# Kernel tuning notes

Measured on AMD Instinct MI355X. Metric: run time of the kernel, lower is better.

Reference implementation:

```python
import jax, jax.numpy as jnp
import numpy as np

N = 50000        # num nodes
E = 800000       # num edges (avg degree 16)
IN_DIM = 64
OUT_DIM = 64
PE_DIM = 24
HEADS = 2
HID = OUT_DIM * HEADS  # 128


def setup_inputs() -> dict:
    key = jax.random.key(0)
    ks = jax.random.split(key, 16)
    std = 0.1  # trunc_normal_(std=0.1) init in the torch module
    return {
        "x": jax.random.normal(ks[0], (N, IN_DIM), jnp.float32),
        "pe_index": jax.random.randint(ks[1], (2, E), 0, N, jnp.int32),
        "pe_val": jax.random.normal(ks[2], (E, PE_DIM), jnp.float32),
        # edge-weight MLP (blocks): input proj, one residual FFN block, final proj
        "W_in": jax.random.normal(ks[3], (PE_DIM, HID), jnp.float32) * std,
        "b_in": jnp.zeros((HID,), jnp.float32),
        "W1": jax.random.normal(ks[4], (HID, HID), jnp.float32) * std,
        "b1": jnp.zeros((HID,), jnp.float32),
        "W2": jax.random.normal(ks[5], (HID, HID), jnp.float32) * std,
        "b2": jnp.zeros((HID,), jnp.float32),
        "W_fin": jax.random.normal(ks[6], (HID, HID), jnp.float32) * std,
        "b_fin": jnp.zeros((HID,), jnp.float32),
        # node feature -> multi-head projection
        "W_x": jax.random.normal(ks[7], (IN_DIM, HID), jnp.float32) * std,
        "b_x": jnp.zeros((HID,), jnp.float32),
        # per-head output bias
        "head_bias": jnp.zeros((1, HEADS, OUT_DIM), jnp.float32),
        # final out projection
        "W_out": jax.random.normal(ks[8], (HID, OUT_DIM), jnp.float32) * std,
        "b_out": jnp.zeros((OUT_DIM,), jnp.float32),
    }


def _edge_mlp(pe, W_in, b_in, W1, b1, W2, b2, W_fin, b_fin):
    # Linear(pe_dim->hid), then residual block [GELU, Linear, GELU, Linear, +res], then Linear(hid->hid)
    g = lambda t: jax.nn.gelu(t, approximate=False)  # torch nn.GELU default = exact erf
    x0 = pe @ W_in + b_in                     # [E, HID]
    h = g(x0) @ W1 + b1
    h = g(h) @ W2 + b2
    x0 = h + x0                               # ResidualLayer: x + x_res
    return x0 @ W_fin + b_fin                 # [E, HID]


def reference(x, pe_index, pe_val, W_in, b_in, W1, b1, W2, b2, W_fin, b_fin,
              W_x, b_x, head_bias, W_out, b_out):
    tgt = pe_index[0]  # messages aggregate to edge_index[0]
    src = pe_index[1]
    score = _edge_mlp(pe_val, W_in, b_in, W1, b1, W2, b2, W_fin, b_fin)
    score = score.reshape(-1, HEADS, OUT_DIM)                 # [E, H, D]
    xh = (x @ W_x + b_x).reshape(-1, HEADS, OUT_DIM)          # [N, H, D]
    msg = xh[src] * score                                     # gather-multiply
    wV = jax.ops.segment_sum(msg, tgt, num_segments=N)        # scatter-add [N, H, D]
    deg = jax.ops.segment_sum(jnp.ones((msg.shape[0],), jnp.float32), tgt, num_segments=N)
    wV = wV / jnp.maximum(deg, 1.0)[:, None, None]            # average=True -> mean aggregation
    h = (wV + head_bias).reshape(-1, HEADS * OUT_DIM)
    return h @ W_out + b_out                                  # out_proj: [N, OUT_DIM]
```

## Files before the change

kernel.cpp:

```cpp
#include <hip/hip_runtime.h>
#include <hip/hip_bf16.h>
#include <math.h>

#define NN 50000
#define EE 800000
#define HID 128
#define PED 24
#define IND 64
#define OUTD 64
#define EBLK 64
#define AKS 136

typedef short bf16x8 __attribute__((ext_vector_type(8)));
typedef float f32x4 __attribute__((ext_vector_type(4)));

__device__ __forceinline__ float gelu_fast(float x) {
    float z = fabsf(x) * 0.70710678118654752440f;
    float t = __builtin_amdgcn_rcpf(1.0f + 0.3275911f * z);
    float poly = t * (0.254829592f +
                 t * (-0.284496736f +
                 t * (1.421413741f +
                 t * (-1.453152027f +
                 t * 1.061405429f))));
    float e = __expf(-z * z);
    float erfa = 1.0f - poly * e;
    float s = copysignf(erfa, x);
    return 0.5f * x * (1.0f + s);
}
__device__ __forceinline__ unsigned short f2bf(float f) {
    unsigned int u = __float_as_uint(f);
    u = (u + 0x7fffu + ((u >> 16) & 1u)) >> 16;
    return (unsigned short)u;
}
__device__ __forceinline__ unsigned int pkbf2(float a, float b) {
    __hip_bfloat162 h = __float22bfloat162_rn(make_float2(a, b));
    return *reinterpret_cast<unsigned int*>(&h);
}
__device__ __forceinline__ float bflo(unsigned int u) {
    return __uint_as_float(u << 16);
}
__device__ __forceinline__ float bfhi(unsigned int u) {
    return __uint_as_float(u & 0xffff0000u);
}

__global__ __launch_bounds__(256) void xh_kernel(
    const float* __restrict__ x, const float* __restrict__ W_x,
    const float* __restrict__ b_x, unsigned short* __restrict__ xhb) {
    int gid = blockIdx.x * 256 + threadIdx.x;
    int n = gid >> 5;
    int q = gid & 31;
    if (n >= NN) return;
    const float* xr = x + (size_t)n * IND;
    float4 acc = *(const float4*)&b_x[q * 4];
#pragma unroll 8
    for (int k = 0; k < IND; k++) {
        float xk = xr[k];
        float4 w = *(const float4*)&W_x[k * HID + q * 4];
        acc.x += xk * w.x; acc.y += xk * w.y;
        acc.z += xk * w.z; acc.w += xk * w.w;
    }
    uint2 p;
    p.x = pkbf2(acc.x, acc.y);
    p.y = pkbf2(acc.z, acc.w);
    ((uint2*)&xhb[(size_t)n * HID])[q] = p;
}

__global__ __launch_bounds__(256) void prep_kernel(
    const float* __restrict__ W_in, const float* __restrict__ W1,
    const float* __restrict__ W2, const float* __restrict__ Wf,
    unsigned short* __restrict__ WT_in, unsigned short* __restrict__ WT1,
    unsigned short* __restrict__ WT2, unsigned short* __restrict__ WTf) {
    int idx = blockIdx.x * 256 + threadIdx.x;
    if (idx < 4096) {
        int j = idx >> 5, k = idx & 31;
        WT_in[idx] = f2bf(k < PED ? W_in[k * HID + j] : 0.f);
    } else if (idx < 4096 + 16384) {
        int i = idx - 4096; int j = i >> 7, k = i & 127;
        WT1[i] = f2bf(W1[k * HID + j]);
    } else if (idx < 4096 + 32768) {
        int i = idx - 4096 - 16384; int j = i >> 7, k = i & 127;
        WT2[i] = f2bf(W2[k * HID + j]);
    } else if (idx < 4096 + 49152) {
        int i = idx - 4096 - 32768; int j = i >> 7, k = i & 127;
        WTf[i] = f2bf(Wf[k * HID + j]);
    }
}

__global__ __launch_bounds__(256) void hist_kernel(const int* __restrict__ pe_idx,
                                                   int* __restrict__ cnt) {
    int e = blockIdx.x * 256 + threadIdx.x;
    if (e < EE) atomicAdd(&cnt[pe_idx[e]], 1);
}

__global__ __launch_bounds__(1024) void scan_kernel(const int* __restrict__ cnt,
                                                    int* __restrict__ woff) {
    __shared__ int s_w[16];
    int tid = threadIdx.x;
    const int chunk = (NN + 1023) / 1024;
    int base = tid * chunk;
    int end = base + chunk; if (end > NN) end = NN;
    int s = 0;
    for (int i = base; i < end; i++) s += cnt[i];
    int v = s;
    int lane = tid & 63, wid = tid >> 6;
#pragma unroll
    for (int d = 1; d < 64; d <<= 1) {
        int u = __shfl_up(v, d, 64);
        if (lane >= d) v += u;
    }
    if (lane == 63) s_w[wid] = v;
    __syncthreads();
    if (tid < 16) {
        int wv = s_w[tid];
#pragma unroll
        for (int d = 1; d < 16; d <<= 1) {
            int u = __shfl_up(wv, d, 64);
            if (tid >= d) wv += u;
        }
        s_w[tid] = wv;
    }
    __syncthreads();
    int exc = v - s + (wid ? s_w[wid - 1] : 0);
    int run = exc;
    for (int i = base; i < end; i++) { woff[i] = run; run += cnt[i]; }
}

__global__ __launch_bounds__(256) void scatter_kernel(const int* __restrict__ pe_idx,
                                                      int* __restrict__ woff,
                                                      int* __restrict__ perm) {
    int e = blockIdx.x * 256 + threadIdx.x;
    if (e < EE) {
        int t = pe_idx[e];
        int p = atomicAdd(&woff[t], 1);
        perm[p] = e;
    }
}

__global__ __launch_bounds__(256, 3) void edge_kernel(
    const float* __restrict__ pe_val, const int* __restrict__ pe_idx,
    const int* __restrict__ perm, const unsigned short* __restrict__ xhb,
    const unsigned short* __restrict__ WT_in, const unsigned short* __restrict__ WT1,
    const unsigned short* __restrict__ WT2, const unsigned short* __restrict__ WTf,
    const float* __restrict__ b_in, const float* __restrict__ b1,
    const float* __restrict__ b2, const float* __restrict__ bfin,
    float* __restrict__ wV) {
    __shared__ unsigned short s_act[EBLK][AKS];
    __shared__ __align__(16) unsigned short s_W[HID][AKS];
    __shared__ int s_eid[EBLK], s_tgt[EBLK], s_src[EBLK];
    float* s_msg = (float*)&s_W[0][0];

    const int tid = threadIdx.x;
    const int lane = tid & 63;
    const int w = tid >> 6;
    const int l15 = lane & 15;
    const int quad = lane >> 4;
    const long b0 = (long)blockIdx.x * EBLK;

    if (tid < EBLK) {
        int eid = perm[b0 + tid];
        s_eid[tid] = eid;
        s_tgt[tid] = pe_idx[eid];
        s_src[tid] = pe_idx[EE + eid];
    }
#pragma unroll
    for (int i = 0; i < 8; i++) {
        int idx = tid + i * 256; int r = idx >> 4, seg = idx & 15;
        *(uint4*)&s_W[r][seg * 8] = *(const uint4*)&WT1[r * HID + seg * 8];
    }
    __syncthreads();
#pragma unroll
    for (int i = 0; i < 8; i++) {
        int idx = tid + i * 256; int e = idx >> 5, k = idx & 31;
        float v = (k < PED) ? pe_val[(size_t)s_eid[e] * PED + k] : 0.f;
        s_act[e][k] = f2bf(v);
    }
    __syncthreads();

    f32x4 C[2][4];
    f32x4 x0s[2][4];
    const f32x4 z4 = {0.f, 0.f, 0.f, 0.f};

    {
        bf16x8 a0 = *(const bf16x8*)&WT_in[((2 * w + 0) * 16 + l15) * 32 + quad * 8];
        bf16x8 a1 = *(const bf16x8*)&WT_in[((2 * w + 1) * 16 + l15) * 32 + quad * 8];
#pragma unroll
        for (int u = 0; u < 4; u++) {
            bf16x8 bfr = *(const bf16x8*)&s_act[u * 16 + l15][quad * 8];
            C[0][u] = __builtin_amdgcn_mfma_f32_16x16x32_bf16(a0, bfr, z4, 0, 0, 0);
            C[1][u] = __builtin_amdgcn_mfma_f32_16x16x32_bf16(a1, bfr, z4, 0, 0, 0);
        }
    }
    __syncthreads();
#pragma unroll
    for (int t = 0; t < 2; t++) {
        int ch0 = (2 * w + t) * 16 + quad * 4;
        float4 bb = *(const float4*)&b_in[ch0];
#pragma unroll
        for (int u = 0; u < 4; u++) {
            int e = u * 16 + l15;
            f32x4 c = C[t][u];
            c[0] += bb.x; c[1] += bb.y; c[2] += bb.z; c[3] += bb.w;
            x0s[t][u] = c;
            uint2 p;
            p.x = pkbf2(gelu_fast(c[0]), gelu_fast(c[1]));
            p.y = pkbf2(gelu_fast(c[2]), gelu_fast(c[3]));
            *(uint2*)&s_act[e][ch0] = p;
        }
    }
    __syncthreads();

#define GEMM128()                                                              \
    {                                                                          \
        _Pragma("unroll") for (int t = 0; t < 2; t++)                          \
            _Pragma("unroll") for (int u = 0; u < 4; u++) C[t][u] = z4;        \
        _Pragma("unroll") for (int ks = 0; ks < 4; ks++) {                     \
            bf16x8 a0 = *(const bf16x8*)&s_W[(2 * w + 0) * 16 + l15]           \
                                            [ks * 32 + quad * 8];              \
            bf16x8 a1 = *(const bf16x8*)&s_W[(2 * w + 1) * 16 + l15]           \
                                            [ks * 32 + quad * 8];              \
            _Pragma("unroll") for (int u = 0; u < 4; u++) {                    \
                bf16x8 bfr = *(const bf16x8*)&s_act[u * 16 + l15]              \
                                                   [ks * 32 + quad * 8];       \
                C[0][u] = __builtin_amdgcn_mfma_f32_16x16x32_bf16(a0, bfr,     \
                                                                  C[0][u], 0, 0, 0); \
                C[1][u] = __builtin_amdgcn_mfma_f32_16x16x32_bf16(a1, bfr,     \
                                                                  C[1][u], 0, 0, 0); \
            }                                                                  \
        }                                                                      \
    }

#define STAGE_W(WT)                                                            \
    _Pragma("unroll") for (int i = 0; i < 8; i++) {                            \
        int idx = tid + i * 256; int r = idx >> 4, seg = idx & 15;             \
        *(uint4*)&s_W[r][seg * 8] = *(const uint4*)&(WT)[r * HID + seg * 8];   \
    }

    GEMM128();
    __syncthreads();
#pragma unroll
    for (int t = 0; t < 2; t++) {
        int ch0 = (2 * w + t) * 16 + quad * 4;
        float4 bb = *(const float4*)&b1[ch0];
#pragma unroll
        for (int u = 0; u < 4; u++) {
            int e = u * 16 + l15;
            f32x4 c = C[t][u];
            uint2 p;
            p.x = pkbf2(gelu_fast(c[0] + bb.x), gelu_fast(c[1] + bb.y));
            p.y = pkbf2(gelu_fast(c[2] + bb.z), gelu_fast(c[3] + bb.w));
            *(uint2*)&s_act[e][ch0] = p;
        }
    }
    STAGE_W(WT2);
    __syncthreads();

    GEMM128();
    __syncthreads();
#pragma unroll
    for (int t = 0; t < 2; t++) {
        int ch0 = (2 * w + t) * 16 + quad * 4;
        float4 bb = *(const float4*)&b2[ch0];
#pragma unroll
        for (int u = 0; u < 4; u++) {
            int e = u * 16 + l15;
            f32x4 c = C[t][u];
            f32x4 x0 = x0s[t][u];
            uint2 p;
            p.x = pkbf2(c[0] + bb.x + x0[0], c[1] + bb.y + x0[1]);
            p.y = pkbf2(c[2] + bb.z + x0[2], c[3] + bb.w + x0[3]);
            *(uint2*)&s_act[e][ch0] = p;
        }
    }
    STAGE_W(WTf);
    __syncthreads();

    GEMM128();
    __syncthreads();
#pragma unroll
    for (int t = 0; t < 2; t++) {
        int ch0 = (2 * w + t) * 16 + quad * 4;
        float4 bb = *(const float4*)&bfin[ch0];
#pragma unroll
        for (int u = 0; u < 4; u++) {
            int e = u * 16 + l15;
            f32x4 c = C[t][u];
            uint2 p;
            p.x = pkbf2(c[0] + bb.x, c[1] + bb.y);
            p.y = pkbf2(c[2] + bb.z, c[3] + bb.w);
            *(uint2*)&s_act[e][ch0] = p;
        }
    }
    __syncthreads();

#pragma unroll
    for (int i = 0; i < 8; i++) {
        int idx = tid + i * 256;
        int e = idx >> 5, c4 = idx & 31;
        int src = s_src[e];
        uint2 xv = ((const uint2*)&xhb[(size_t)src * HID])[c4];
        uint2 sv = *(const uint2*)&s_act[e][c4 * 4];
        float4 m;
        m.x = bflo(xv.x) * bflo(sv.x);
        m.y = bfhi(xv.x) * bfhi(sv.x);
        m.z = bflo(xv.y) * bflo(sv.y);
        m.w = bfhi(xv.y) * bfhi(sv.y);
        *(float4*)&s_msg[e * HID + c4 * 4] = m;
    }
    __syncthreads();

    {
        const int h = tid >> 7;
        const int c = tid & 127;
        const int e0h = h * 32;
        float acc = 0.f;
        int prev = s_tgt[e0h];
        bool firstseg = true;
        for (int e = e0h; e < e0h + 32; e++) {
            int t = s_tgt[e];
            if (t != prev) {
                if (firstseg) atomicAdd(&wV[(size_t)prev * HID + c], acc);
                else          wV[(size_t)prev * HID + c] = acc;
                firstseg = false;
                acc = 0.f;
                prev = t;
            }
            acc += s_msg[e * HID + c];
        }
        atomicAdd(&wV[(size_t)prev * HID + c], acc);
    }
#undef GEMM128
#undef STAGE_W
}

__global__ __launch_bounds__(256) void out_kernel(
    const float* __restrict__ wV, const int* __restrict__ cnt,
    const float* __restrict__ head_bias, const float* __restrict__ W_out,
    const float* __restrict__ b_out, float* __restrict__ out) {
    int gid = blockIdx.x * 256 + threadIdx.x;
    int n = gid >> 4;
    int q = gid & 15;
    if (n >= NN) return;
    float inv = 1.0f / fmaxf((float)cnt[n], 1.0f);
    const float* wr = wV + (size_t)n * HID;
    float4 acc = *(const float4*)&b_out[q * 4];
#pragma unroll 4
    for (int k = 0; k < HID; k++) {
        float hv = wr[k] * inv + head_bias[k];
        float4 wv4 = *(const float4*)&W_out[k * OUTD + q * 4];
        acc.x += hv * wv4.x; acc.y += hv * wv4.y;
        acc.z += hv * wv4.z; acc.w += hv * wv4.w;
    }
    *(float4*)&out[(size_t)n * OUTD + q * 4] = acc;
}

extern "C" void kernel_launch(void* const* d_in, const int* in_sizes, int n_in,
                              void* d_out, int out_size, void* d_ws, size_t ws_size,
                              hipStream_t stream) {
    const float* x      = (const float*)d_in[0];
    const int*   pe_idx = (const int*)d_in[1];
    const float* pe_val = (const float*)d_in[2];
    const float* W_in   = (const float*)d_in[3];
    const float* b_in   = (const float*)d_in[4];
    const float* W1     = (const float*)d_in[5];
    const float* b1     = (const float*)d_in[6];
    const float* W2     = (const float*)d_in[7];
    const float* b2     = (const float*)d_in[8];
    const float* Wf     = (const float*)d_in[9];
    const float* bfin   = (const float*)d_in[10];
    const float* W_x    = (const float*)d_in[11];
    const float* b_x    = (const float*)d_in[12];
    const float* hb     = (const float*)d_in[13];
    const float* W_out  = (const float*)d_in[14];
    const float* b_out  = (const float*)d_in[15];
    float* out = (float*)d_out;

    float* wV   = (float*)d_ws;
    int*   cnt  = (int*)(wV + (size_t)NN * HID);
    int*   woff = cnt + NN;
    int*   perm = woff + NN;
    unsigned short* WT_in = (unsigned short*)(perm + EE);
    unsigned short* WT1   = WT_in + 128 * 32;
    unsigned short* WT2   = WT1 + 128 * 128;
    unsigned short* WTf   = WT2 + 128 * 128;
    unsigned short* xhb   = WTf + 128 * 128;

    hipMemsetAsync(wV, 0, ((size_t)NN * HID + NN) * sizeof(float), stream);

    hist_kernel<<<(EE + 255) / 256, 256, 0, stream>>>(pe_idx, cnt);
    scan_kernel<<<1, 1024, 0, stream>>>(cnt, woff);
    scatter_kernel<<<(EE + 255) / 256, 256, 0, stream>>>(pe_idx, woff, perm);
    prep_kernel<<<208, 256, 0, stream>>>(W_in, W1, W2, Wf, WT_in, WT1, WT2, WTf);
    xh_kernel<<<(NN * 32 + 255) / 256, 256, 0, stream>>>(x, W_x, b_x, xhb);

    edge_kernel<<<EE / EBLK, 256, 0, stream>>>(pe_val, pe_idx, perm, xhb,
                                               WT_in, WT1, WT2, WTf,
                                               b_in, b1, b2, bfin, wV);

    out_kernel<<<(NN * 16 + 255) / 256, 256, 0, stream>>>(wV, cnt, hb, W_out,
                                                          b_out, out);
}
```

Before: 697.8 us.

## Double edge tile to 128 with 512 threads and merge preprocessing kernels

The edge kernel now handles 128 edges per block with 8 waves. Pairs of waves share channel slices and split the edges, so each staged weight matrix in shared memory is reused across twice as many edges. The message and segment-reduce phase runs in two halves of 64 edges to fit the shared buffer, and that phase adds extra barriers with only half the threads active in the reduction. Separately, the histogram, weight-transpose and xh projection kernels are fused into one launch, which removes two launches.

```diff
diff --git a/kernel.cpp b/kernel.cpp
--- a/kernel.cpp
+++ b/kernel.cpp
@@ -8,7 +8,7 @@
 #define PED 24
 #define IND 64
 #define OUTD 64
-#define EBLK 64
+#define EBLK 128
 #define AKS 136
 
 typedef short bf16x8 __attribute__((ext_vector_type(8)));
@@ -43,53 +43,55 @@
     return __uint_as_float(u & 0xffff0000u);
 }
 
-__global__ __launch_bounds__(256) void xh_kernel(
-    const float* __restrict__ x, const float* __restrict__ W_x,
-    const float* __restrict__ b_x, unsigned short* __restrict__ xhb) {
-    int gid = blockIdx.x * 256 + threadIdx.x;
-    int n = gid >> 5;
-    int q = gid & 31;
-    if (n >= NN) return;
-    const float* xr = x + (size_t)n * IND;
-    float4 acc = *(const float4*)&b_x[q * 4];
-#pragma unroll 8
-    for (int k = 0; k < IND; k++) {
-        float xk = xr[k];
-        float4 w = *(const float4*)&W_x[k * HID + q * 4];
-        acc.x += xk * w.x; acc.y += xk * w.y;
-        acc.z += xk * w.z; acc.w += xk * w.w;
-    }
-    uint2 p;
-    p.x = pkbf2(acc.x, acc.y);
-    p.y = pkbf2(acc.z, acc.w);
-    ((uint2*)&xhb[(size_t)n * HID])[q] = p;
-}
-
-__global__ __launch_bounds__(256) void prep_kernel(
+#define HB 3125
+#define PB 208
+#define XB 6250
+__global__ __launch_bounds__(256) void pre_kernel(
+    const int* __restrict__ pe_idx, int* __restrict__ cnt,
     const float* __restrict__ W_in, const float* __restrict__ W1,
     const float* __restrict__ W2, const float* __restrict__ Wf,
     unsigned short* __restrict__ WT_in, unsigned short* __restrict__ WT1,
-    unsigned short* __restrict__ WT2, unsigned short* __restrict__ WTf) {
-    int idx = blockIdx.x * 256 + threadIdx.x;
-    if (idx < 4096) {
-        int j = idx >> 5, k = idx & 31;
-        WT_in[idx] = f2bf(k < PED ? W_in[k * HID + j] : 0.f);
-    } else if (idx < 4096 + 16384) {
-        int i = idx - 4096; int j = i >> 7, k = i & 127;
-        WT1[i] = f2bf(W1[k * HID + j]);
-    } else if (idx < 4096 + 32768) {
-        int i = idx - 4096 - 16384; int j = i >> 7, k = i & 127;
-        WT2[i] = f2bf(W2[k * HID + j]);
-    } else if (idx < 4096 + 49152) {
-        int i = idx - 4096 - 32768; int j = i >> 7, k = i & 127;
-        WTf[i] = f2bf(Wf[k * HID + j]);
-    }
-}
-
-__global__ __launch_bounds__(256) void hist_kernel(const int* __restrict__ pe_idx,
-                                                   int* __restrict__ cnt) {
-    int e = blockIdx.x * 256 + threadIdx.x;
-    if (e < EE) atomicAdd(&cnt[pe_idx[e]], 1);
+    unsigned short* __restrict__ WT2, unsigned short* __restrict__ WTf,
+    const float* __restrict__ x, const float* __restrict__ W_x,
+    const float* __restrict__ b_x, unsigned short* __restrict__ xhb) {
+    int b = blockIdx.x;
+    int tid = threadIdx.x;
+    if (b < HB) {
+        int e = b * 256 + tid;
+        atomicAdd(&cnt[pe_idx[e]], 1);
+    } else if (b < HB + PB) {
+        int idx = (b - HB) * 256 + tid;
+        if (idx < 4096) {
+            int j = idx >> 5, k = idx & 31;
+            WT_in[idx] = f2bf(k < PED ? W_in[k * HID + j] : 0.f);
+        } else if (idx < 4096 + 16384) {
+            int i = idx - 4096; int j = i >> 7, k = i & 127;
+            WT1[i] = f2bf(W1[k * HID + j]);
+        } else if (idx < 4096 + 32768) {
+            int i = idx - 4096 - 16384; int j = i >> 7, k = i & 127;
+            WT2[i] = f2bf(W2[k * HID + j]);
+        } else {
+            int i = idx - 4096 - 32768; int j = i >> 7, k = i & 127;
+            WTf[i] = f2bf(Wf[k * HID + j]);
+        }
+    } else {
+        int gid = (b - HB - PB) * 256 + tid;
+        int n = gid >> 5;
+        int q = gid & 31;
+        const float* xr = x + (size_t)n * IND;
+        float4 acc = *(const float4*)&b_x[q * 4];
+#pragma unroll 8
+        for (int k = 0; k < IND; k++) {
+            float xk = xr[k];
+            float4 w = *(const float4*)&W_x[k * HID + q * 4];
+            acc.x += xk * w.x; acc.y += xk * w.y;
+            acc.z += xk * w.z; acc.w += xk * w.w;
+        }
+        uint2 p;
+        p.x = pkbf2(acc.x, acc.y);
+        p.y = pkbf2(acc.z, acc.w);
+        ((uint2*)&xhb[(size_t)n * HID])[q] = p;
+    }
 }
 
 __global__ __launch_bounds__(1024) void scan_kernel(const int* __restrict__ cnt,
@@ -136,7 +138,7 @@
     }
 }
 
-__global__ __launch_bounds__(256, 3) void edge_kernel(
+__global__ __launch_bounds__(512, 4) void edge_kernel(
     const float* __restrict__ pe_val, const int* __restrict__ pe_idx,
     const int* __restrict__ perm, const unsigned short* __restrict__ xhb,
     const unsigned short* __restrict__ WT_in, const unsigned short* __restrict__ WT1,
@@ -154,6 +156,8 @@
     const int w = tid >> 6;
     const int l15 = lane & 15;
     const int quad = lane >> 4;
+    const int chp = w & 3;
+    const int ehb = (w >> 2) * 4;
     const long b0 = (long)blockIdx.x * EBLK;
 
     if (tid < EBLK) {
@@ -163,14 +167,14 @@
         s_src[tid] = pe_idx[EE + eid];
     }
 #pragma unroll
+    for (int i = 0; i < 4; i++) {
+        int idx = tid + i * 512; int r = idx >> 4, seg = idx & 15;
+        *(uint4*)&s_W[r][seg * 8] = *(const uint4*)&WT1[r * HID + seg * 8];
+    }
+    __syncthreads();
+#pragma unroll
     for (int i = 0; i < 8; i++) {
-        int idx = tid + i * 256; int r = idx >> 4, seg = idx & 15;
-        *(uint4*)&s_W[r][seg * 8] = *(const uint4*)&WT1[r * HID + seg * 8];
-    }
-    __syncthreads();
-#pragma unroll
-    for (int i = 0; i < 8; i++) {
-        int idx = tid + i * 256; int e = idx >> 5, k = idx & 31;
+        int idx = tid + i * 512; int e = idx >> 5, k = idx & 31;
         float v = (k < PED) ? pe_val[(size_t)s_eid[e] * PED + k] : 0.f;
         s_act[e][k] = f2bf(v);
     }
@@ -181,11 +185,11 @@
     const f32x4 z4 = {0.f, 0.f, 0.f, 0.f};
 
     {
-        bf16x8 a0 = *(const bf16x8*)&WT_in[((2 * w + 0) * 16 + l15) * 32 + quad * 8];
-        bf16x8 a1 = *(const bf16x8*)&WT_in[((2 * w + 1) * 16 + l15) * 32 + quad * 8];
+        bf16x8 a0 = *(const bf16x8*)&WT_in[((2 * chp + 0) * 16 + l15) * 32 + quad * 8];
+        bf16x8 a1 = *(const bf16x8*)&WT_in[((2 * chp + 1) * 16 + l15) * 32 + quad * 8];
 #pragma unroll
         for (int u = 0; u < 4; u++) {
-            bf16x8 bfr = *(const bf16x8*)&s_act[u * 16 + l15][quad * 8];
+            bf16x8 bfr = *(const bf16x8*)&s_act[(ehb + u) * 16 + l15][quad * 8];
             C[0][u] = __builtin_amdgcn_mfma_f32_16x16x32_bf16(a0, bfr, z4, 0, 0, 0);
             C[1][u] = __builtin_amdgcn_mfma_f32_16x16x32_bf16(a1, bfr, z4, 0, 0, 0);
         }
@@ -193,11 +197,11 @@
     __syncthreads();
 #pragma unroll
     for (int t = 0; t < 2; t++) {
-        int ch0 = (2 * w + t) * 16 + quad * 4;
+        int ch0 = (2 * chp + t) * 16 + quad * 4;
         float4 bb = *(const float4*)&b_in[ch0];
 #pragma unroll
         for (int u = 0; u < 4; u++) {
-            int e = u * 16 + l15;
+            int e = (ehb + u) * 16 + l15;
             f32x4 c = C[t][u];
             c[0] += bb.x; c[1] += bb.y; c[2] += bb.z; c[3] += bb.w;
             x0s[t][u] = c;
@@ -214,12 +218,12 @@
         _Pragma("unroll") for (int t = 0; t < 2; t++)                          \
             _Pragma("unroll") for (int u = 0; u < 4; u++) C[t][u] = z4;        \
         _Pragma("unroll") for (int ks = 0; ks < 4; ks++) {                     \
-            bf16x8 a0 = *(const bf16x8*)&s_W[(2 * w + 0) * 16 + l15]           \
+            bf16x8 a0 = *(const bf16x8*)&s_W[(2 * chp + 0) * 16 + l15]         \
                                             [ks * 32 + quad * 8];              \
-            bf16x8 a1 = *(const bf16x8*)&s_W[(2 * w + 1) * 16 + l15]           \
+            bf16x8 a1 = *(const bf16x8*)&s_W[(2 * chp + 1) * 16 + l15]         \
                                             [ks * 32 + quad * 8];              \
             _Pragma("unroll") for (int u = 0; u < 4; u++) {                    \
-                bf16x8 bfr = *(const bf16x8*)&s_act[u * 16 + l15]              \
+                bf16x8 bfr = *(const bf16x8*)&s_act[(ehb + u) * 16 + l15]      \
                                                    [ks * 32 + quad * 8];       \
                 C[0][u] = __builtin_amdgcn_mfma_f32_16x16x32_bf16(a0, bfr,     \
                                                                   C[0][u], 0, 0, 0); \
@@ -230,8 +234,8 @@
     }
 
 #define STAGE_W(WT)                                                            \
-    _Pragma("unroll") for (int i = 0; i < 8; i++) {                            \
-        int idx = tid + i * 256; int r = idx >> 4, seg = idx & 15;             \
+    _Pragma("unroll") for (int i = 0; i < 4; i++) {                            \
+        int idx = tid + i * 512; int r = idx >> 4, seg = idx & 15;             \
         *(uint4*)&s_W[r][seg * 8] = *(const uint4*)&(WT)[r * HID + seg * 8];   \
     }
 
@@ -239,11 +243,11 @@
     __syncthreads();
 #pragma unroll
     for (int t = 0; t < 2; t++) {
-        int ch0 = (2 * w + t) * 16 + quad * 4;
+        int ch0 = (2 * chp + t) * 16 + quad * 4;
         float4 bb = *(const float4*)&b1[ch0];
 #pragma unroll
         for (int u = 0; u < 4; u++) {
-            int e = u * 16 + l15;
+            int e = (ehb + u) * 16 + l15;
             f32x4 c = C[t][u];
             uint2 p;
             p.x = pkbf2(gelu_fast(c[0] + bb.x), gelu_fast(c[1] + bb.y));
@@ -258,11 +262,11 @@
     __syncthreads();
 #pragma unroll
     for (int t = 0; t < 2; t++) {
-        int ch0 = (2 * w + t) * 16 + quad * 4;
+        int ch0 = (2 * chp + t) * 16 + quad * 4;
         float4 bb = *(const float4*)&b2[ch0];
 #pragma unroll
         for (int u = 0; u < 4; u++) {
-            int e = u * 16 + l15;
+            int e = (ehb + u) * 16 + l15;
             f32x4 c = C[t][u];
             f32x4 x0 = x0s[t][u];
             uint2 p;
@@ -278,11 +282,11 @@
     __syncthreads();
 #pragma unroll
     for (int t = 0; t < 2; t++) {
-        int ch0 = (2 * w + t) * 16 + quad * 4;
+        int ch0 = (2 * chp + t) * 16 + quad * 4;
         float4 bb = *(const float4*)&bfin[ch0];
 #pragma unroll
         for (int u = 0; u < 4; u++) {
-            int e = u * 16 + l15;
+            int e = (ehb + u) * 16 + l15;
             f32x4 c = C[t][u];
             uint2 p;
             p.x = pkbf2(c[0] + bb.x, c[1] + bb.y);
@@ -292,41 +296,45 @@
     }
     __syncthreads();
 
-#pragma unroll
-    for (int i = 0; i < 8; i++) {
-        int idx = tid + i * 256;
-        int e = idx >> 5, c4 = idx & 31;
-        int src = s_src[e];
-        uint2 xv = ((const uint2*)&xhb[(size_t)src * HID])[c4];
-        uint2 sv = *(const uint2*)&s_act[e][c4 * 4];
-        float4 m;
-        m.x = bflo(xv.x) * bflo(sv.x);
-        m.y = bfhi(xv.x) * bfhi(sv.x);
-        m.z = bflo(xv.y) * bflo(sv.y);
-        m.w = bfhi(xv.y) * bfhi(sv.y);
-        *(float4*)&s_msg[e * HID + c4 * 4] = m;
-    }
-    __syncthreads();
-
-    {
-        const int h = tid >> 7;
-        const int c = tid & 127;
-        const int e0h = h * 32;
-        float acc = 0.f;
-        int prev = s_tgt[e0h];
-        bool firstseg = true;
-        for (int e = e0h; e < e0h + 32; e++) {
-            int t = s_tgt[e];
-            if (t != prev) {
-                if (firstseg) atomicAdd(&wV[(size_t)prev * HID + c], acc);
-                else          wV[(size_t)prev * HID + c] = acc;
-                firstseg = false;
-                acc = 0.f;
-                prev = t;
+#pragma unroll 1
+    for (int h = 0; h < 2; h++) {
+#pragma unroll
+        for (int i = 0; i < 4; i++) {
+            int idx = tid + i * 512;
+            int el = idx >> 5, c4 = idx & 31;
+            int e = h * 64 + el;
+            int src = s_src[e];
+            uint2 xv = ((const uint2*)&xhb[(size_t)src * HID])[c4];
+            uint2 sv = *(const uint2*)&s_act[e][c4 * 4];
+            float4 m;
+            m.x = bflo(xv.x) * bflo(sv.x);
+            m.y = bfhi(xv.x) * bfhi(sv.x);
+            m.z = bflo(xv.y) * bflo(sv.y);
+            m.w = bfhi(xv.y) * bfhi(sv.y);
+            *(float4*)&s_msg[el * HID + c4 * 4] = m;
+        }
+        __syncthreads();
+        if (tid < 256) {
+            const int sub = tid >> 7;
+            const int c = tid & 127;
+            const int e0 = h * 64 + sub * 32;
+            float acc = 0.f;
+            int prev = s_tgt[e0];
+            bool firstseg = true;
+            for (int e = e0; e < e0 + 32; e++) {
+                int t = s_tgt[e];
+                if (t != prev) {
+                    if (firstseg) atomicAdd(&wV[(size_t)prev * HID + c], acc);
+                    else          wV[(size_t)prev * HID + c] = acc;
+                    firstseg = false;
+                    acc = 0.f;
+                    prev = t;
+                }
+                acc += s_msg[(e - h * 64) * HID + c];
             }
-            acc += s_msg[e * HID + c];
-        }
-        atomicAdd(&wV[(size_t)prev * HID + c], acc);
+            atomicAdd(&wV[(size_t)prev * HID + c], acc);
+        }
+        __syncthreads();
     }
 #undef GEMM128
 #undef STAGE_W
@@ -386,13 +394,13 @@
 
     hipMemsetAsync(wV, 0, ((size_t)NN * HID + NN) * sizeof(float), stream);
 
-    hist_kernel<<<(EE + 255) / 256, 256, 0, stream>>>(pe_idx, cnt);
+    pre_kernel<<<HB + PB + XB, 256, 0, stream>>>(
+        pe_idx, cnt, W_in, W1, W2, Wf, WT_in, WT1, WT2, WTf,
+        x, W_x, b_x, xhb);
     scan_kernel<<<1, 1024, 0, stream>>>(cnt, woff);
     scatter_kernel<<<(EE + 255) / 256, 256, 0, stream>>>(pe_idx, woff, perm);
-    prep_kernel<<<208, 256, 0, stream>>>(W_in, W1, W2, Wf, WT_in, WT1, WT2, WTf);
-    xh_kernel<<<(NN * 32 + 255) / 256, 256, 0, stream>>>(x, W_x, b_x, xhb);
-
-    edge_kernel<<<EE / EBLK, 256, 0, stream>>>(pe_val, pe_idx, perm, xhb,
+
+    edge_kernel<<<EE / EBLK, 512, 0, stream>>>(pe_val, pe_idx, perm, xhb,
                                                WT_in, WT1, WT2, WTf,
                                                b_in, b1, b2, bfin, wV);
 
```

New measurement: 726.4 us. 4.1% more time.
